# Kernel tuning notes

Hardware: AMD Instinct MI355X
Metric: run time of the kernel (lower is better)

## Reference

```python
import jax, jax.numpy as jnp
import numpy as np

B, S, E, H, NW, FFN = 16384, 8, 8, 8, 8, 512  # seq==num_heads, embed==n_wires per view() constraint
EPS = 1e-5


def _layer_norm(x, g, b):
    m = x.mean(-1, keepdims=True)
    v = ((x - m) ** 2).mean(-1, keepdims=True)
    return (x - m) / jnp.sqrt(v + EPS) * g + b


def _ring_cnot_z(c):
    # c: [..., NW] = cos(theta) per wire for a product RX state.
    # CNOT(0,1),(1,2),...,(NW-2,NW-1),(NW-1,0) => z_w -> prefix-XOR; Z-expectations factorize:
    # <Z_w> = prod_{j<=w} c_j (w>=1);  <Z_0> = prod_{j>=1} c_j
    cp = jnp.cumprod(c, axis=-1)
    z0 = jnp.prod(c[..., 1:], axis=-1, keepdims=True)
    return jnp.concatenate([z0, cp[..., 1:]], axis=-1)


def setup_inputs() -> dict:
    key = jax.random.key(0)
    ks = jax.random.split(key, 14)
    rn = lambda k, shp, s=0.1: jax.random.normal(k, shp, jnp.float32) * s
    return {
        "x": jax.random.normal(ks[0], (B, S, E), jnp.float32),
        "in_proj_w": rn(ks[1], (3 * E, E)), "in_proj_b": rn(ks[2], (3 * E,)),
        "out_proj_w": rn(ks[3], (E, E)), "out_proj_b": rn(ks[4], (E,)),
        "rx_attn": rn(ks[5], (NW,), 1.0),
        "combine_w": rn(ks[6], (E, E)), "combine_b": rn(ks[7], (E,)),
        "ln1_g": jnp.ones((E,), jnp.float32), "ln1_b": jnp.zeros((E,), jnp.float32),
        "rx_ffn": rn(ks[8], (NW,), 1.0),
        "lin1_w": rn(ks[9], (FFN, NW)), "lin1_b": rn(ks[10], (FFN,)),
        "lin2_w": rn(ks[11], (E, FFN)), "lin2_b": rn(ks[12], (E,)),
        "ln2_g": jnp.ones((E,), jnp.float32), "ln2_b": jnp.zeros((E,), jnp.float32),
    }


def _forward(x, in_proj_w, in_proj_b, out_proj_w, out_proj_b, rx_attn,
             combine_w, combine_b, ln1_g, ln1_b, rx_ffn,
             lin1_w, lin1_b, lin2_w, lin2_b, ln2_g, ln2_b):
    dk = E // H
    # --- nn.MultiheadAttention (self-attn, batch_first, eval/no-dropout) ---
    qkv = x @ in_proj_w.T + in_proj_b                      # [B,S,3E]
    q, k, v = jnp.split(qkv, 3, axis=-1)
    to_h = lambda t: t.reshape(B, S, H, dk).transpose(0, 2, 1, 3)   # [B,H,S,dk]
    scores = jnp.einsum('bhqd,bhkd->bhqk', to_h(q), to_h(k)) / np.float32(np.sqrt(dk))
    a = jax.nn.softmax(scores, axis=-1)
    o = jnp.einsum('bhqk,bhkd->bhqd', a, to_h(v)).transpose(0, 2, 1, 3).reshape(B, S, E)
    attn_out = o @ out_proj_w.T + out_proj_b               # [B,S,E]

    # --- per-head quantum circuit: RX(feature) + RX(param) per wire, CNOT ring, PauliZ ---
    theta = attn_out[:, :H, :NW] + rx_attn                 # head i = seq slot i; feature j -> wire j
    q_out = _ring_cnot_z(jnp.cos(theta)).reshape(B, S, E)  # [B,H,NW] -> [B,S,E]
    q_out = q_out @ combine_w.T + combine_b
    attn_total = (attn_out + q_out) @ combine_w.T + combine_b  # combine applied twice, as in source

    h = _layer_norm(x + attn_total, ln1_g, ln1_b)

    # --- per-token quantum FFN: RX(feature)+RX(param), PauliZ (no entanglers) => cos(theta) ---
    zf = jnp.cos(h[..., :NW] + rx_ffn)                     # [B,S,NW]
    u = jax.nn.relu(zf @ lin1_w.T + lin1_b)                # [B,S,FFN]
    ffn_out = u @ lin2_w.T + lin2_b                        # [B,S,E]

    return _layer_norm(h + ffn_out, ln2_g, ln2_b)


def reference(x, in_proj_w, in_proj_b, out_proj_w, out_proj_b, rx_attn,
              combine_w, combine_b, ln1_g, ln1_b, rx_ffn,
              lin1_w, lin1_b, lin2_w, lin2_b, ln2_g, ln2_b):
    return _forward(x, in_proj_w, in_proj_b, out_proj_w, out_proj_b, rx_attn,
                    combine_w, combine_b, ln1_g, ln1_b, rx_ffn,
                    lin1_w, lin1_b, lin2_w, lin2_b, ln2_g, ln2_b)
```

## Files before the change

### kernel.cpp

```cpp
#include <hip/hip_runtime.h>


typedef __fp16 half2v __attribute__((ext_vector_type(2)));
typedef __fp16 half4  __attribute__((ext_vector_type(4)));
typedef float  float4v __attribute__((ext_vector_type(4)));

#define SWZ16(v) __int_as_float(__builtin_amdgcn_ds_swizzle(__float_as_int(v), (16 << 10) | 0x1F))
#define SWZI_(v, dlit) __builtin_amdgcn_ds_swizzle((v), ((dlit) << 5) | 0x18)
#define GATHERJ8(dst, src)                                  \
    do {                                                    \
        dst[0] = SWZI_(src, 0); dst[1] = SWZI_(src, 1);     \
        dst[2] = SWZI_(src, 2); dst[3] = SWZI_(src, 3);     \
        dst[4] = SWZI_(src, 4); dst[5] = SWZI_(src, 5);     \
        dst[6] = SWZI_(src, 6); dst[7] = SWZI_(src, 7);     \
    } while (0)

#define O_RXA 0
#define O_G1  16
#define O_B1  32
#define O_RXF 48
#define O_L2B 64
#define O_G2  80
#define O_B2  96

__global__ __launch_bounds__(512, 4) void tbq_fused(
    const float* __restrict__ x,
    const float* __restrict__ ipw, const float* __restrict__ ipb,
    const float* __restrict__ opw, const float* __restrict__ opb,
    const float* __restrict__ rxa,
    const float* __restrict__ cw,  const float* __restrict__ cb,
    const float* __restrict__ g1,  const float* __restrict__ b1,
    const float* __restrict__ rxf,
    const float* __restrict__ l1w, const float* __restrict__ l1b,
    const float* __restrict__ l2w, const float* __restrict__ l2b,
    const float* __restrict__ g2,  const float* __restrict__ b2,
    float* __restrict__ out)
{
    __shared__ half4 a1l[2048];
    __shared__ half4 a2l[2048];
    __shared__ half4 frontA[320];
    __shared__ __align__(16) float wl[112];

    const int tid = threadIdx.x;
    const int l   = tid & 63;
    const int wv  = tid >> 6;
    const int n   = l & 15;
    const int g   = l >> 4;
    const int k0  = g * 4;
    const int gtok = blockIdx.x * 128 + wv * 16;

    float4 xw = make_float4(0.f, 0.f, 0.f, 0.f);
    if (g < 2) xw = *reinterpret_cast<const float4*>(x + (gtok + n) * 8 + k0);

    const half4 zh = {(__fp16)0.f, (__fp16)0.f, (__fp16)0.f, (__fp16)0.f};

    if (tid < 320) {
        const int t = tid >> 6, ll = tid & 63;
        const int m = ll & 15, kk0 = (ll >> 4) * 4;
        half4 r = zh;
        if (m < 8) {
            const float* Wp = (t == 0) ? ipw : (t == 1) ? ipw + 64 :
                              (t == 2) ? ipw + 128 : (t == 3) ? opw : cw;
            const float* Bp = (t == 0) ? ipb : (t == 1) ? ipb + 8 :
                              (t == 2) ? ipb + 16 : (t == 3) ? opb : cb;
            #pragma unroll
            for (int j = 0; j < 4; ++j) {
                int k = kk0 + j;
                float v = (k < 8) ? Wp[m * 8 + k] : ((k == 8) ? Bp[m] : 0.f);
                r[j] = (__fp16)v;
            }
        }
        frontA[tid] = r;
    } else if (tid < 432) {
        const int p = (tid - 320) >> 4, i = (tid - 320) & 15;
        float v = 0.f;
        if (i < 8) {
            v = (p == 0) ? rxa[i] : (p == 1) ? g1[i] : (p == 2) ? b1[i] :
                (p == 3) ? rxf[i] : (p == 4) ? l2b[i] : (p == 5) ? g2[i] : b2[i];
        }
        wl[p * 16 + i] = v;
    }
    #pragma unroll 1
    for (int i = 0; i < 4; ++i) {
        const int u  = tid + i * 512;
        const int nf = u >> 6, ll = u & 63;
        const int mm = ll & 15, kk0 = (ll >> 4) * 4;
        half4 r1 = zh;
        if (ll < 32) {
            float4 w = *reinterpret_cast<const float4*>(l1w + (nf * 16 + mm) * 8 + kk0);
            half2v c0 = __builtin_amdgcn_cvt_pkrtz(w.x, w.y);
            half2v c1 = __builtin_amdgcn_cvt_pkrtz(w.z, w.w);
            r1.x = c0.x; r1.y = c0.y; r1.z = c1.x; r1.w = c1.y;
        } else if (ll < 48) {
            r1.x = (__fp16)l1b[nf * 16 + mm];
        }
        a1l[u] = r1;
        half4 r2 = zh;
        if (mm < 8) {
            float4 w = *reinterpret_cast<const float4*>(l2w + mm * 512 + nf * 16 + kk0);
            half2v c0 = __builtin_amdgcn_cvt_pkrtz(w.x, w.y);
            half2v c1 = __builtin_amdgcn_cvt_pkrtz(w.z, w.w);
            r2.x = c0.x; r2.y = c0.y; r2.z = c1.x; r2.w = c1.y;
        }
        a2l[u] = r2;
    }
    __syncthreads();

    half4 bx = zh;
    if (g < 2) {
        half2v p0 = __builtin_amdgcn_cvt_pkrtz(xw.x, xw.y);
        half2v p1 = __builtin_amdgcn_cvt_pkrtz(xw.z, xw.w);
        bx.x = p0.x; bx.y = p0.y; bx.z = p1.x; bx.w = p1.y;
    } else if (g == 2) bx.x = (__fp16)1.f;

    half4 Aq = frontA[l],       Ak = frontA[64 + l], Av = frontA[128 + l];
    half4 Ao = frontA[192 + l], Ac = frontA[256 + l];

    const float4v zero4 = {0.f, 0.f, 0.f, 0.f};
    float4v qf = __builtin_amdgcn_mfma_f32_16x16x16f16(Aq, bx, zero4, 0, 0, 0);
    float4v kf = __builtin_amdgcn_mfma_f32_16x16x16f16(Ak, bx, zero4, 0, 0, 0);
    float4v vf = __builtin_amdgcn_mfma_f32_16x16x16f16(Av, bx, zero4, 0, 0, 0);

    float orow[4];
    #pragma unroll
    for (int r = 0; r < 4; ++r) {
        half2v pk = __builtin_amdgcn_cvt_pkrtz(kf[r], vf[r]);
        int kvp = __builtin_bit_cast(int, pk);
        int kvg[8];
        GATHERJ8(kvg, kvp);
        const float qh2 = qf[r] * 1.44269504f;
        float sum = 0.f, ov = 0.f;
        #pragma unroll
        for (int j = 0; j < 8; ++j) {
            half2v kv = __builtin_bit_cast(half2v, kvg[j]);
            float p = exp2f(qh2 * (float)kv.x);
            sum += p;
            ov = fmaf(p, (float)kv.y, ov);
        }
        orow[r] = ov * __builtin_amdgcn_rcpf(sum);
    }

    half4 bo = zh;
    if (g < 2) {
        half2v p0 = __builtin_amdgcn_cvt_pkrtz(orow[0], orow[1]);
        half2v p1 = __builtin_amdgcn_cvt_pkrtz(orow[2], orow[3]);
        bo.x = p0.x; bo.y = p0.y; bo.z = p1.x; bo.w = p1.y;
    } else if (g == 2) bo.x = (__fp16)1.f;
    float4v aof = __builtin_amdgcn_mfma_f32_16x16x16f16(Ao, bo, zero4, 0, 0, 0);

    const float4 rxa4 = *reinterpret_cast<const float4*>(&wl[O_RXA + k0]);
    float cx0 = __cosf(aof[0] + rxa4.x), cx1 = __cosf(aof[1] + rxa4.y);
    float cx2 = __cosf(aof[2] + rxa4.z), cx3 = __cosf(aof[3] + rxa4.w);
    float ct0 = SWZ16(cx0), ct1 = SWZ16(cx1), ct2 = SWZ16(cx2), ct3 = SWZ16(cx3);
    const bool sel = (g == 0);
    float cc[8];
    cc[0] = sel ? cx0 : ct0; cc[1] = sel ? cx1 : ct1;
    cc[2] = sel ? cx2 : ct2; cc[3] = sel ? cx3 : ct3;
    cc[4] = sel ? ct0 : cx0; cc[5] = sel ? ct1 : cx1;
    cc[6] = sel ? ct2 : cx2; cc[7] = sel ? ct3 : cx3;
    float z8[8];
    {
        float run = cc[0];
        #pragma unroll
        for (int w = 1; w < 8; ++w) { run *= cc[w]; z8[w] = run; }
        float s17 = cc[1];
        #pragma unroll
        for (int w = 2; w < 8; ++w) s17 *= cc[w];
        z8[0] = s17;
    }

    float zs0 = sel ? z8[0] : z8[4], zs1 = sel ? z8[1] : z8[5];
    float zs2 = sel ? z8[2] : z8[6], zs3 = sel ? z8[3] : z8[7];
    half4 bz1 = zh;
    if (g < 2) {
        half2v p0 = __builtin_amdgcn_cvt_pkrtz(zs0, zs1);
        half2v p1 = __builtin_amdgcn_cvt_pkrtz(zs2, zs3);
        bz1.x = p0.x; bz1.y = p0.y; bz1.z = p1.x; bz1.w = p1.y;
    } else if (g == 2) bz1.x = (__fp16)1.f;
    float4v qo = __builtin_amdgcn_mfma_f32_16x16x16f16(Ac, bz1, zero4, 0, 0, 0);
    float4v saqf = aof + qo;

    half4 bs = zh;
    if (g < 2) {
        half2v p0 = __builtin_amdgcn_cvt_pkrtz(saqf[0], saqf[1]);
        half2v p1 = __builtin_amdgcn_cvt_pkrtz(saqf[2], saqf[3]);
        bs.x = p0.x; bs.y = p0.y; bs.z = p1.x; bs.w = p1.y;
    } else if (g == 2) bs.x = (__fp16)1.f;
    float4v atf = __builtin_amdgcn_mfma_f32_16x16x16f16(Ac, bs, zero4, 0, 0, 0);

    float r10 = xw.x + atf[0], r11 = xw.y + atf[1];
    float r12 = xw.z + atf[2], r13 = xw.w + atf[3];
    float s4 = (r10 + r11) + (r12 + r13);
    float mean = (s4 + SWZ16(s4)) * 0.125f;
    float dv0 = r10 - mean, dv1 = r11 - mean, dv2 = r12 - mean, dv3 = r13 - mean;
    float vq = (dv0 * dv0 + dv1 * dv1) + (dv2 * dv2 + dv3 * dv3);
    float var = (vq + SWZ16(vq)) * 0.125f;
    float rs = __builtin_amdgcn_rsqf(var + 1e-5f);
    const float4 g14 = *reinterpret_cast<const float4*>(&wl[O_G1 + k0]);
    const float4 b14 = *reinterpret_cast<const float4*>(&wl[O_B1 + k0]);
    float hh0 = fmaf(dv0 * rs, g14.x, b14.x);
    float hh1 = fmaf(dv1 * rs, g14.y, b14.y);
    float hh2 = fmaf(dv2 * rs, g14.z, b14.z);
    float hh3 = fmaf(dv3 * rs, g14.w, b14.w);

    const float4 rxf4 = *reinterpret_cast<const float4*>(&wl[O_RXF + k0]);
    half4 bz = zh;
    if (g < 2) {
        half2v p0 = __builtin_amdgcn_cvt_pkrtz(__cosf(hh0 + rxf4.x), __cosf(hh1 + rxf4.y));
        half2v p1 = __builtin_amdgcn_cvt_pkrtz(__cosf(hh2 + rxf4.z), __cosf(hh3 + rxf4.w));
        bz.x = p0.x; bz.y = p0.y; bz.z = p1.x; bz.w = p1.y;
    } else if (g == 2) bz.x = (__fp16)1.f;

    float4v acc = zero4;
    #pragma unroll 4
    for (int nf = 0; nf < 32; ++nf) {
        half4 a1f = a1l[nf * 64 + l];
        half4 a2f = a2l[nf * 64 + l];
        float4v d = __builtin_amdgcn_mfma_f32_16x16x16f16(a1f, bz, zero4, 0, 0, 0);
        half2v p0 = __builtin_amdgcn_cvt_pkrtz(d[0], d[1]);
        half2v p1 = __builtin_amdgcn_cvt_pkrtz(d[2], d[3]);
        half4 bu; bu.x = p0.x; bu.y = p0.y; bu.z = p1.x; bu.w = p1.y;
        bu = __builtin_elementwise_max(bu, zh);
        acc = __builtin_amdgcn_mfma_f32_16x16x16f16(a2f, bu, acc, 0, 0, 0);
    }

    if (g < 2) {
        const float4 lb4 = *reinterpret_cast<const float4*>(&wl[O_L2B + k0]);
        const float4 g24 = *reinterpret_cast<const float4*>(&wl[O_G2 + k0]);
        const float4 b24 = *reinterpret_cast<const float4*>(&wl[O_B2 + k0]);
        float r20 = hh0 + acc[0] + lb4.x;
        float r21 = hh1 + acc[1] + lb4.y;
        float r22 = hh2 + acc[2] + lb4.z;
        float r23 = hh3 + acc[3] + lb4.w;
        float part = (r20 + r21) + (r22 + r23);
        float mean2 = (part + SWZ16(part)) * 0.125f;
        float e0 = r20 - mean2, e1 = r21 - mean2, e2 = r22 - mean2, e3 = r23 - mean2;
        float vp = (e0 * e0 + e1 * e1) + (e2 * e2 + e3 * e3);
        float rs2 = __builtin_amdgcn_rsqf((vp + SWZ16(vp)) * 0.125f + 1e-5f);
        float4 o;
        o.x = fmaf(e0 * rs2, g24.x, b24.x);
        o.y = fmaf(e1 * rs2, g24.y, b24.y);
        o.z = fmaf(e2 * rs2, g24.z, b24.z);
        o.w = fmaf(e3 * rs2, g24.w, b24.w);
        *reinterpret_cast<float4*>(out + (gtok + n) * 8 + k0) = o;
    }
}

extern "C" void kernel_launch(void* const* d_in, const int* in_sizes, int n_in,
                              void* d_out, int out_size, void* d_ws, size_t ws_size,
                              hipStream_t stream) {
    const float* x   = (const float*)d_in[0];
    const float* ipw = (const float*)d_in[1];
    const float* ipb = (const float*)d_in[2];
    const float* opw = (const float*)d_in[3];
    const float* opb = (const float*)d_in[4];
    const float* rxa = (const float*)d_in[5];
    const float* cw  = (const float*)d_in[6];
    const float* cb  = (const float*)d_in[7];
    const float* g1  = (const float*)d_in[8];
    const float* b1  = (const float*)d_in[9];
    const float* rxf = (const float*)d_in[10];
    const float* l1w = (const float*)d_in[11];
    const float* l1b = (const float*)d_in[12];
    const float* l2w = (const float*)d_in[13];
    const float* l2b = (const float*)d_in[14];
    const float* g2  = (const float*)d_in[15];
    const float* b2  = (const float*)d_in[16];
    float* out = (float*)d_out;

    const int tokens = 16384 * 8;
    tbq_fused<<<dim3(tokens / 128), dim3(512), 0, stream>>>(
        x, ipw, ipb, opw, opb, rxa, cw, cb, g1, b1, rxf,
        l1w, l1b, l2w, l2b, g2, b2, out);
}
```

Before: 21.23 us.

## Process two 16-token tiles per wave to reuse FFN weight fragments

Each wave now handles 32 tokens (two 16-token MFMA tiles) instead of 16, so the grid is halved. The per-block LDS weight staging and the a1l/a2l fragment loads in the FFN loop are amortized over twice as many tokens, and the two independent MFMA chains can interleave. The cost is more registers per thread and half as many blocks, which may reduce occupancy and latency hiding.

```diff
diff --git a/kernel.cpp b/kernel.cpp
--- a/kernel.cpp
+++ b/kernel.cpp
@@ -47,10 +47,14 @@
     const int n   = l & 15;
     const int g   = l >> 4;
     const int k0  = g * 4;
-    const int gtok = blockIdx.x * 128 + wv * 16;
-
-    float4 xw = make_float4(0.f, 0.f, 0.f, 0.f);
-    if (g < 2) xw = *reinterpret_cast<const float4*>(x + (gtok + n) * 8 + k0);
+    const int base0 = blockIdx.x * 256 + wv * 32;
+
+    float4 xw[2];
+    xw[0] = make_float4(0.f, 0.f, 0.f, 0.f); xw[1] = xw[0];
+    if (g < 2) {
+        xw[0] = *reinterpret_cast<const float4*>(x + (base0 + n) * 8 + k0);
+        xw[1] = *reinterpret_cast<const float4*>(x + (base0 + 16 + n) * 8 + k0);
+    }
 
     const half4 zh = {(__fp16)0.f, (__fp16)0.f, (__fp16)0.f, (__fp16)0.f};
 
@@ -106,143 +110,171 @@
     }
     __syncthreads();
 
-    half4 bx = zh;
-    if (g < 2) {
-        half2v p0 = __builtin_amdgcn_cvt_pkrtz(xw.x, xw.y);
-        half2v p1 = __builtin_amdgcn_cvt_pkrtz(xw.z, xw.w);
-        bx.x = p0.x; bx.y = p0.y; bx.z = p1.x; bx.w = p1.y;
-    } else if (g == 2) bx.x = (__fp16)1.f;
-
     half4 Aq = frontA[l],       Ak = frontA[64 + l], Av = frontA[128 + l];
     half4 Ao = frontA[192 + l], Ac = frontA[256 + l];
-
     const float4v zero4 = {0.f, 0.f, 0.f, 0.f};
-    float4v qf = __builtin_amdgcn_mfma_f32_16x16x16f16(Aq, bx, zero4, 0, 0, 0);
-    float4v kf = __builtin_amdgcn_mfma_f32_16x16x16f16(Ak, bx, zero4, 0, 0, 0);
-    float4v vf = __builtin_amdgcn_mfma_f32_16x16x16f16(Av, bx, zero4, 0, 0, 0);
-
-    float orow[4];
+
+    half4 bx[2]; bx[0] = zh; bx[1] = zh;
     #pragma unroll
-    for (int r = 0; r < 4; ++r) {
-        half2v pk = __builtin_amdgcn_cvt_pkrtz(kf[r], vf[r]);
-        int kvp = __builtin_bit_cast(int, pk);
-        int kvg[8];
-        GATHERJ8(kvg, kvp);
-        const float qh2 = qf[r] * 1.44269504f;
-        float sum = 0.f, ov = 0.f;
+    for (int t = 0; t < 2; ++t) {
+        if (g < 2) {
+            half2v p0 = __builtin_amdgcn_cvt_pkrtz(xw[t].x, xw[t].y);
+            half2v p1 = __builtin_amdgcn_cvt_pkrtz(xw[t].z, xw[t].w);
+            bx[t].x = p0.x; bx[t].y = p0.y; bx[t].z = p1.x; bx[t].w = p1.y;
+        } else if (g == 2) bx[t].x = (__fp16)1.f;
+    }
+
+    float4v qf[2], kf[2], vf[2];
+    #pragma unroll
+    for (int t = 0; t < 2; ++t) {
+        qf[t] = __builtin_amdgcn_mfma_f32_16x16x16f16(Aq, bx[t], zero4, 0, 0, 0);
+        kf[t] = __builtin_amdgcn_mfma_f32_16x16x16f16(Ak, bx[t], zero4, 0, 0, 0);
+        vf[t] = __builtin_amdgcn_mfma_f32_16x16x16f16(Av, bx[t], zero4, 0, 0, 0);
+    }
+
+    half4 bzf[2]; bzf[0] = zh; bzf[1] = zh;
+    float hhv[2][4];
+    const bool sel = (g == 0);
+    const float4 rxa4 = *reinterpret_cast<const float4*>(&wl[O_RXA + k0]);
+    const float4 g14  = *reinterpret_cast<const float4*>(&wl[O_G1 + k0]);
+    const float4 b14  = *reinterpret_cast<const float4*>(&wl[O_B1 + k0]);
+    const float4 rxf4 = *reinterpret_cast<const float4*>(&wl[O_RXF + k0]);
+
+    #pragma unroll
+    for (int t = 0; t < 2; ++t) {
+        float orow[4];
         #pragma unroll
-        for (int j = 0; j < 8; ++j) {
-            half2v kv = __builtin_bit_cast(half2v, kvg[j]);
-            float p = exp2f(qh2 * (float)kv.x);
-            sum += p;
-            ov = fmaf(p, (float)kv.y, ov);
-        }
-        orow[r] = ov * __builtin_amdgcn_rcpf(sum);
-    }
-
-    half4 bo = zh;
-    if (g < 2) {
-        half2v p0 = __builtin_amdgcn_cvt_pkrtz(orow[0], orow[1]);
-        half2v p1 = __builtin_amdgcn_cvt_pkrtz(orow[2], orow[3]);
-        bo.x = p0.x; bo.y = p0.y; bo.z = p1.x; bo.w = p1.y;
-    } else if (g == 2) bo.x = (__fp16)1.f;
-    float4v aof = __builtin_amdgcn_mfma_f32_16x16x16f16(Ao, bo, zero4, 0, 0, 0);
-
-    const float4 rxa4 = *reinterpret_cast<const float4*>(&wl[O_RXA + k0]);
-    float cx0 = __cosf(aof[0] + rxa4.x), cx1 = __cosf(aof[1] + rxa4.y);
-    float cx2 = __cosf(aof[2] + rxa4.z), cx3 = __cosf(aof[3] + rxa4.w);
-    float ct0 = SWZ16(cx0), ct1 = SWZ16(cx1), ct2 = SWZ16(cx2), ct3 = SWZ16(cx3);
-    const bool sel = (g == 0);
-    float cc[8];
-    cc[0] = sel ? cx0 : ct0; cc[1] = sel ? cx1 : ct1;
-    cc[2] = sel ? cx2 : ct2; cc[3] = sel ? cx3 : ct3;
-    cc[4] = sel ? ct0 : cx0; cc[5] = sel ? ct1 : cx1;
-    cc[6] = sel ? ct2 : cx2; cc[7] = sel ? ct3 : cx3;
-    float z8[8];
-    {
-        float run = cc[0];
-        #pragma unroll
-        for (int w = 1; w < 8; ++w) { run *= cc[w]; z8[w] = run; }
-        float s17 = cc[1];
-        #pragma unroll
-        for (int w = 2; w < 8; ++w) s17 *= cc[w];
-        z8[0] = s17;
-    }
-
-    float zs0 = sel ? z8[0] : z8[4], zs1 = sel ? z8[1] : z8[5];
-    float zs2 = sel ? z8[2] : z8[6], zs3 = sel ? z8[3] : z8[7];
-    half4 bz1 = zh;
-    if (g < 2) {
-        half2v p0 = __builtin_amdgcn_cvt_pkrtz(zs0, zs1);
-        half2v p1 = __builtin_amdgcn_cvt_pkrtz(zs2, zs3);
-        bz1.x = p0.x; bz1.y = p0.y; bz1.z = p1.x; bz1.w = p1.y;
-    } else if (g == 2) bz1.x = (__fp16)1.f;
-    float4v qo = __builtin_amdgcn_mfma_f32_16x16x16f16(Ac, bz1, zero4, 0, 0, 0);
-    float4v saqf = aof + qo;
-
-    half4 bs = zh;
-    if (g < 2) {
-        half2v p0 = __builtin_amdgcn_cvt_pkrtz(saqf[0], saqf[1]);
-        half2v p1 = __builtin_amdgcn_cvt_pkrtz(saqf[2], saqf[3]);
-        bs.x = p0.x; bs.y = p0.y; bs.z = p1.x; bs.w = p1.y;
-    } else if (g == 2) bs.x = (__fp16)1.f;
-    float4v atf = __builtin_amdgcn_mfma_f32_16x16x16f16(Ac, bs, zero4, 0, 0, 0);
-
-    float r10 = xw.x + atf[0], r11 = xw.y + atf[1];
-    float r12 = xw.z + atf[2], r13 = xw.w + atf[3];
-    float s4 = (r10 + r11) + (r12 + r13);
-    float mean = (s4 + SWZ16(s4)) * 0.125f;
-    float dv0 = r10 - mean, dv1 = r11 - mean, dv2 = r12 - mean, dv3 = r13 - mean;
-    float vq = (dv0 * dv0 + dv1 * dv1) + (dv2 * dv2 + dv3 * dv3);
-    float var = (vq + SWZ16(vq)) * 0.125f;
-    float rs = __builtin_amdgcn_rsqf(var + 1e-5f);
-    const float4 g14 = *reinterpret_cast<const float4*>(&wl[O_G1 + k0]);
-    const float4 b14 = *reinterpret_cast<const float4*>(&wl[O_B1 + k0]);
-    float hh0 = fmaf(dv0 * rs, g14.x, b14.x);
-    float hh1 = fmaf(dv1 * rs, g14.y, b14.y);
-    float hh2 = fmaf(dv2 * rs, g14.z, b14.z);
-    float hh3 = fmaf(dv3 * rs, g14.w, b14.w);
-
-    const float4 rxf4 = *reinterpret_cast<const float4*>(&wl[O_RXF + k0]);
-    half4 bz = zh;
-    if (g < 2) {
-        half2v p0 = __builtin_amdgcn_cvt_pkrtz(__cosf(hh0 + rxf4.x), __cosf(hh1 + rxf4.y));
-        half2v p1 = __builtin_amdgcn_cvt_pkrtz(__cosf(hh2 + rxf4.z), __cosf(hh3 + rxf4.w));
-        bz.x = p0.x; bz.y = p0.y; bz.z = p1.x; bz.w = p1.y;
-    } else if (g == 2) bz.x = (__fp16)1.f;
-
-    float4v acc = zero4;
-    #pragma unroll 4
+        for (int r = 0; r < 4; ++r) {
+            half2v pk = __builtin_amdgcn_cvt_pkrtz(kf[t][r], vf[t][r]);
+            int kvp = __builtin_bit_cast(int, pk);
+            int kvg[8];
+            GATHERJ8(kvg, kvp);
+            const float qh2 = qf[t][r] * 1.44269504f;
+            float sum = 0.f, ov = 0.f;
+            #pragma unroll
+            for (int j = 0; j < 8; ++j) {
+                half2v kv = __builtin_bit_cast(half2v, kvg[j]);
+                float p = exp2f(qh2 * (float)kv.x);
+                sum += p;
+                ov = fmaf(p, (float)kv.y, ov);
+            }
+            orow[r] = ov * __builtin_amdgcn_rcpf(sum);
+        }
+
+        half4 bo = zh;
+        if (g < 2) {
+            half2v p0 = __builtin_amdgcn_cvt_pkrtz(orow[0], orow[1]);
+            half2v p1 = __builtin_amdgcn_cvt_pkrtz(orow[2], orow[3]);
+            bo.x = p0.x; bo.y = p0.y; bo.z = p1.x; bo.w = p1.y;
+        } else if (g == 2) bo.x = (__fp16)1.f;
+        float4v aof = __builtin_amdgcn_mfma_f32_16x16x16f16(Ao, bo, zero4, 0, 0, 0);
+
+        float cx0 = __cosf(aof[0] + rxa4.x), cx1 = __cosf(aof[1] + rxa4.y);
+        float cx2 = __cosf(aof[2] + rxa4.z), cx3 = __cosf(aof[3] + rxa4.w);
+        float ct0 = SWZ16(cx0), ct1 = SWZ16(cx1), ct2 = SWZ16(cx2), ct3 = SWZ16(cx3);
+        float cc[8];
+        cc[0] = sel ? cx0 : ct0; cc[1] = sel ? cx1 : ct1;
+        cc[2] = sel ? cx2 : ct2; cc[3] = sel ? cx3 : ct3;
+        cc[4] = sel ? ct0 : cx0; cc[5] = sel ? ct1 : cx1;
+        cc[6] = sel ? ct2 : cx2; cc[7] = sel ? ct3 : cx3;
+        float z8[8];
+        {
+            float run = cc[0];
+            #pragma unroll
+            for (int w = 1; w < 8; ++w) { run *= cc[w]; z8[w] = run; }
+            float s17 = cc[1];
+            #pragma unroll
+            for (int w = 2; w < 8; ++w) s17 *= cc[w];
+            z8[0] = s17;
+        }
+
+        float zs0 = sel ? z8[0] : z8[4], zs1 = sel ? z8[1] : z8[5];
+        float zs2 = sel ? z8[2] : z8[6], zs3 = sel ? z8[3] : z8[7];
+        half4 bz1 = zh;
+        if (g < 2) {
+            half2v p0 = __builtin_amdgcn_cvt_pkrtz(zs0, zs1);
+            half2v p1 = __builtin_amdgcn_cvt_pkrtz(zs2, zs3);
+            bz1.x = p0.x; bz1.y = p0.y; bz1.z = p1.x; bz1.w = p1.y;
+        } else if (g == 2) bz1.x = (__fp16)1.f;
+        float4v qo = __builtin_amdgcn_mfma_f32_16x16x16f16(Ac, bz1, zero4, 0, 0, 0);
+        float4v saqf = aof + qo;
+
+        half4 bs = zh;
+        if (g < 2) {
+            half2v p0 = __builtin_amdgcn_cvt_pkrtz(saqf[0], saqf[1]);
+            half2v p1 = __builtin_amdgcn_cvt_pkrtz(saqf[2], saqf[3]);
+            bs.x = p0.x; bs.y = p0.y; bs.z = p1.x; bs.w = p1.y;
+        } else if (g == 2) bs.x = (__fp16)1.f;
+        float4v atf = __builtin_amdgcn_mfma_f32_16x16x16f16(Ac, bs, zero4, 0, 0, 0);
+
+        float r10 = xw[t].x + atf[0], r11 = xw[t].y + atf[1];
+        float r12 = xw[t].z + atf[2], r13 = xw[t].w + atf[3];
+        float s4 = (r10 + r11) + (r12 + r13);
+        float mean = (s4 + SWZ16(s4)) * 0.125f;
+        float dv0 = r10 - mean, dv1 = r11 - mean, dv2 = r12 - mean, dv3 = r13 - mean;
+        float vq = (dv0 * dv0 + dv1 * dv1) + (dv2 * dv2 + dv3 * dv3);
+        float var = (vq + SWZ16(vq)) * 0.125f;
+        float rs = __builtin_amdgcn_rsqf(var + 1e-5f);
+        hhv[t][0] = fmaf(dv0 * rs, g14.x, b14.x);
+        hhv[t][1] = fmaf(dv1 * rs, g14.y, b14.y);
+        hhv[t][2] = fmaf(dv2 * rs, g14.z, b14.z);
+        hhv[t][3] = fmaf(dv3 * rs, g14.w, b14.w);
+
+        if (g < 2) {
+            half2v p0 = __builtin_amdgcn_cvt_pkrtz(__cosf(hhv[t][0] + rxf4.x),
+                                                   __cosf(hhv[t][1] + rxf4.y));
+            half2v p1 = __builtin_amdgcn_cvt_pkrtz(__cosf(hhv[t][2] + rxf4.z),
+                                                   __cosf(hhv[t][3] + rxf4.w));
+            bzf[t].x = p0.x; bzf[t].y = p0.y; bzf[t].z = p1.x; bzf[t].w = p1.y;
+        } else if (g == 2) bzf[t].x = (__fp16)1.f;
+    }
+
+    float4v acc0 = zero4, acc1 = zero4;
+    #pragma unroll 2
     for (int nf = 0; nf < 32; ++nf) {
         half4 a1f = a1l[nf * 64 + l];
         half4 a2f = a2l[nf * 64 + l];
-        float4v d = __builtin_amdgcn_mfma_f32_16x16x16f16(a1f, bz, zero4, 0, 0, 0);
-        half2v p0 = __builtin_amdgcn_cvt_pkrtz(d[0], d[1]);
-        half2v p1 = __builtin_amdgcn_cvt_pkrtz(d[2], d[3]);
-        half4 bu; bu.x = p0.x; bu.y = p0.y; bu.z = p1.x; bu.w = p1.y;
-        bu = __builtin_elementwise_max(bu, zh);
-        acc = __builtin_amdgcn_mfma_f32_16x16x16f16(a2f, bu, acc, 0, 0, 0);
+        float4v d0 = __builtin_amdgcn_mfma_f32_16x16x16f16(a1f, bzf[0], zero4, 0, 0, 0);
+        float4v d1 = __builtin_amdgcn_mfma_f32_16x16x16f16(a1f, bzf[1], zero4, 0, 0, 0);
+        half4 bu0, bu1;
+        {
+            half2v p0 = __builtin_amdgcn_cvt_pkrtz(d0[0], d0[1]);
+            half2v p1 = __builtin_amdgcn_cvt_pkrtz(d0[2], d0[3]);
+            bu0.x = p0.x; bu0.y = p0.y; bu0.z = p1.x; bu0.w = p1.y;
+            p0 = __builtin_amdgcn_cvt_pkrtz(d1[0], d1[1]);
+            p1 = __builtin_amdgcn_cvt_pkrtz(d1[2], d1[3]);
+            bu1.x = p0.x; bu1.y = p0.y; bu1.z = p1.x; bu1.w = p1.y;
+        }
+        bu0 = __builtin_elementwise_max(bu0, zh);
+        bu1 = __builtin_elementwise_max(bu1, zh);
+        acc0 = __builtin_amdgcn_mfma_f32_16x16x16f16(a2f, bu0, acc0, 0, 0, 0);
+        acc1 = __builtin_amdgcn_mfma_f32_16x16x16f16(a2f, bu1, acc1, 0, 0, 0);
     }
 
     if (g < 2) {
         const float4 lb4 = *reinterpret_cast<const float4*>(&wl[O_L2B + k0]);
         const float4 g24 = *reinterpret_cast<const float4*>(&wl[O_G2 + k0]);
         const float4 b24 = *reinterpret_cast<const float4*>(&wl[O_B2 + k0]);
-        float r20 = hh0 + acc[0] + lb4.x;
-        float r21 = hh1 + acc[1] + lb4.y;
-        float r22 = hh2 + acc[2] + lb4.z;
-        float r23 = hh3 + acc[3] + lb4.w;
-        float part = (r20 + r21) + (r22 + r23);
-        float mean2 = (part + SWZ16(part)) * 0.125f;
-        float e0 = r20 - mean2, e1 = r21 - mean2, e2 = r22 - mean2, e3 = r23 - mean2;
-        float vp = (e0 * e0 + e1 * e1) + (e2 * e2 + e3 * e3);
-        float rs2 = __builtin_amdgcn_rsqf((vp + SWZ16(vp)) * 0.125f + 1e-5f);
-        float4 o;
-        o.x = fmaf(e0 * rs2, g24.x, b24.x);
-        o.y = fmaf(e1 * rs2, g24.y, b24.y);
-        o.z = fmaf(e2 * rs2, g24.z, b24.z);
-        o.w = fmaf(e3 * rs2, g24.w, b24.w);
-        *reinterpret_cast<float4*>(out + (gtok + n) * 8 + k0) = o;
+
+        #pragma unroll
+        for (int t = 0; t < 2; ++t) {
+            float4v acc = t ? acc1 : acc0;
+            float r20 = hhv[t][0] + acc[0] + lb4.x;
+            float r21 = hhv[t][1] + acc[1] + lb4.y;
+            float r22 = hhv[t][2] + acc[2] + lb4.z;
+            float r23 = hhv[t][3] + acc[3] + lb4.w;
+            float part = (r20 + r21) + (r22 + r23);
+            float mean2 = (part + SWZ16(part)) * 0.125f;
+            float e0 = r20 - mean2, e1 = r21 - mean2, e2 = r22 - mean2, e3 = r23 - mean2;
+            float vp = (e0 * e0 + e1 * e1) + (e2 * e2 + e3 * e3);
+            float rs2 = __builtin_amdgcn_rsqf((vp + SWZ16(vp)) * 0.125f + 1e-5f);
+            float4 o;
+            o.x = fmaf(e0 * rs2, g24.x, b24.x);
+            o.y = fmaf(e1 * rs2, g24.y, b24.y);
+            o.z = fmaf(e2 * rs2, g24.z, b24.z);
+            o.w = fmaf(e3 * rs2, g24.w, b24.w);
+            *reinterpret_cast<float4*>(out + (base0 + t * 16 + n) * 8 + k0) = o;
+        }
     }
 }
 
@@ -269,7 +301,7 @@
     float* out = (float*)d_out;
 
     const int tokens = 16384 * 8;
-    tbq_fused<<<dim3(tokens / 128), dim3(512), 0, stream>>>(
+    tbq_fused<<<dim3(tokens / 256), dim3(512), 0, stream>>>(
         x, ipw, ipb, opw, opb, rxa, cw, cb, g1, b1, rxf,
         l1w, l1b, l2w, l2b, g2, b2, out);
 }
```

New measurement: 20.56 us. 1.03x faster.
